# Optimization experiments

Measured on AMD Instinct MI355X. Metric: run time of the kernel, lower is better.

## Reference

```python
import jax, jax.numpy as jnp
import numpy as np

B, JX, JQ, D = 16, 4096, 512, 256
VERY_NEG = -1e30


def setup_inputs() -> dict:
    key = jax.random.key(0)
    ks = jax.random.split(key, 8)
    c = jax.random.normal(ks[0], (B, JX, D), dtype=jnp.float32)
    q = jax.random.normal(ks[1], (B, JQ, D), dtype=jnp.float32)
    # glorot-ish scaled weights for [4d, d] projections
    s = 1.0 / np.sqrt(4 * D)
    Wr = jax.random.normal(ks[2], (4 * D, D), dtype=jnp.float32) * s
    Wg = jax.random.normal(ks[3], (4 * D, D), dtype=jnp.float32) * s
    Br = jnp.zeros((D,), dtype=jnp.float32)
    Bg = jnp.zeros((D,), dtype=jnp.float32)
    # padding masks from random valid lengths (realistic ragged batch)
    c_len = jax.random.randint(ks[4], (B,), JX // 2, JX + 1)
    q_len = jax.random.randint(ks[5], (B,), JQ // 2, JQ + 1)
    c_mask = jnp.arange(JX)[None, :] < c_len[:, None]
    q_mask = jnp.arange(JQ)[None, :] < q_len[:, None]
    return {"c": c, "q": q, "Wr": Wr, "Br": Br, "Wg": Wg, "Bg": Bg,
            "c_mask": c_mask, "q_mask": q_mask}


def reference(c, q, Wr, Br, Wg, Bg, c_mask, q_mask):
    # logits[b,x,j] = <c[b,x], q[b,j]>
    logits = jnp.einsum('bxd,bjd->bxj', c, q)
    # exp_mask: add VERY_NEG where (c_mask & q_mask) is False
    cq_mask = c_mask[:, :, None] & q_mask[:, None, :]  # [B,JX,JQ]
    logits = logits + (1.0 - cq_mask.astype(logits.dtype)) * VERY_NEG
    a = jax.nn.softmax(logits, axis=-1)                # [B,JX,JQ]
    q_a = jnp.einsum('bxj,bjd->bxd', a, q)             # [B,JX,D]
    # semantic fusion unit
    cc = jnp.concatenate([c, q_a, c * q_a, c - q_a], axis=-1)  # [B,JX,4D]
    r_ = jnp.tanh(cc @ Wr + Br)
    g = jax.nn.sigmoid(cc @ Wg + Bg)
    return g * r_ + (1.0 - g) * c
```

## Files before the change

### kernel.cpp

```cpp
#include <hip/hip_runtime.h>
#include <hip/hip_bf16.h>
#include <stdint.h>

#define NB 16
#define JXX 4096
#define JQQ 512
#define DDD 256
#define LOG2E 1.44269504f

typedef __attribute__((ext_vector_type(8))) _Float16 f16x8;
typedef __attribute__((ext_vector_type(4))) _Float16 f16x4;
typedef __attribute__((ext_vector_type(4))) float f32x4;

__device__ __forceinline__ uint16_t f2h(float f) {
    union { _Float16 h; uint16_t s; } u; u.h = (_Float16)f; return u.s;
}
__device__ __forceinline__ float h2f(uint16_t s) {
    union { _Float16 h; uint16_t s; } u; u.s = s; return (float)u.h;
}

__device__ __forceinline__ void gload_lds16(const void* g, void* l) {
    __builtin_amdgcn_global_load_lds(
        (const __attribute__((address_space(1))) void*)g,
        (__attribute__((address_space(3))) void*)l, 16, 0, 0);
}

#define VMW(N) asm volatile("s_waitcnt vmcnt(" #N ")" ::: "memory")

__global__ void k_mask(const void* cmask, const void* qmask,
                       uint8_t* cm8, uint8_t* qm8) {
    int i = blockIdx.x * 256 + threadIdx.x;
    uint32_t w0c = *(const uint32_t*)cmask;
    uint32_t w0q = *(const uint32_t*)qmask;
    int mc = (w0c == 1u) ? 1 : (w0c == 0x3f800000u ? 2 : 0);
    int mq = (w0q == 1u) ? 1 : (w0q == 0x3f800000u ? 2 : 0);
    if (i < NB * JXX) {
        uint8_t v;
        if (mc == 1)      v = ((const int*)cmask)[i] != 0;
        else if (mc == 2) v = ((const float*)cmask)[i] != 0.0f;
        else              v = ((const uint8_t*)cmask)[i] != 0;
        cm8[i] = v;
    }
    if (i < NB * JQQ) {
        uint8_t v;
        if (mq == 1)      v = ((const int*)qmask)[i] != 0;
        else if (mq == 2) v = ((const float*)qmask)[i] != 0.0f;
        else              v = ((const uint8_t*)qmask)[i] != 0;
        qm8[i] = v;
    }
}

__global__ void k_prep_q(const float* __restrict__ qg,
                         uint16_t* __restrict__ qS,
                         uint16_t* __restrict__ qTS) {
    __shared__ float tile[64][65];
    const int b = blockIdx.z, j0 = blockIdx.x * 64, d0 = blockIdx.y * 64;
    const int t = threadIdx.x;
    #pragma unroll
    for (int i = 0; i < 16; i++) {
        int e = t + 256 * i;
        int r = e >> 6, c = e & 63;
        tile[r][c] = qg[((long)b * JQQ + j0 + r) * DDD + d0 + c];
    }
    __syncthreads();
    #pragma unroll
    for (int i = 0; i < 2; i++) {
        int e = t + 256 * i;
        int r = e >> 3, c8 = e & 7;
        f16x8 v;
        #pragma unroll
        for (int k = 0; k < 8; k++) v[k] = (_Float16)tile[r][c8 * 8 + k];
        int jt = (j0 >> 5) + (r >> 5);
        int row = r & 31;
        int d8 = (d0 >> 3) + c8;
        int byt = ((row * 512 + d8 * 16) ^ ((row & 7) << 4));
        *(f16x8*)(qS + ((long)(b * 16 + jt)) * 8192 + (byt >> 1)) = v;
    }
    #pragma unroll
    for (int i = 0; i < 2; i++) {
        int e = t + 256 * i;
        int dd = e >> 3, j8 = e & 7;
        f16x8 v;
        #pragma unroll
        for (int k = 0; k < 8; k++) v[k] = (_Float16)tile[j8 * 8 + k][dd];
        int jt = (j0 >> 5) + (j8 >> 2);
        int d = d0 + dd;
        int byt = ((d * 64 + (j8 & 3) * 16) ^ (((d >> 1) & 3) << 4));
        *(f16x8*)(qTS + ((long)(b * 16 + jt)) * 8192 + (byt >> 1)) = v;
    }
}

__global__ void k_prep_w(const float* __restrict__ Wr, const float* __restrict__ Wg,
                         uint16_t* __restrict__ WP2) {
    __shared__ _Float16 tile[32 * 264];
    const int rg = blockIdx.y;
    const float* W = rg ? Wg : Wr;
    const int kt = blockIdx.x, t = threadIdx.x;
    #pragma unroll
    for (int i = 0; i < 32; i++) {
        int e = t + 256 * i;
        int r = e >> 8, c = e & 255;
        tile[r * 264 + c] = (_Float16)W[(long)(kt * 32 + r) * 256 + c];
    }
    __syncthreads();
    const int step = (kt & 7) * 4 + (kt >> 3);
    #pragma unroll
    for (int ss = 0; ss < 4; ss++) {
        int slot = ss * 256 + t;
        int ntg = slot >> 6, lane = slot & 63;
        int gg = lane >> 4, l = lane & 15;
        f16x8 v;
        #pragma unroll
        for (int i = 0; i < 8; i++) v[i] = tile[(gg * 8 + i) * 264 + ntg * 16 + l];
        int hh = ntg >> 3, ntl = ntg & 7;
        long off = (long)step * 16384 + hh * 8192 + rg * 4096 + ntl * 512 + lane * 8;
        *(f16x8*)(WP2 + off) = v;
    }
}

__global__ __launch_bounds__(256, 2) void k_attn(
    const float* __restrict__ cg,
    const uint16_t* __restrict__ qS,
    const uint16_t* __restrict__ qTS,
    const uint8_t* __restrict__ cm8,
    const uint8_t* __restrict__ qm8,
    uint16_t* __restrict__ qa16,
    uint16_t* __restrict__ c16)
{
    __shared__ __align__(16) uint16_t qbuf[2][8192];
    __shared__ __align__(16) uint16_t qTbuf[2][8192];
    __shared__ __align__(16) uint16_t P_lds[4 * 32 * 40];
    __shared__ __align__(16) uint32_t qm_lds[128];

    const int b = blockIdx.y;
    const int t = threadIdx.x;
    const int wave = t >> 6;
    const int lane = t & 63;
    const int l15 = lane & 15;
    const int g = lane >> 4;
    const int xw = blockIdx.x * 128 + wave * 32;

    if (t < 128) {
        uint32_t m = ((const uint32_t*)(qm8 + (long)b * JQQ))[t];
        qm_lds[t] = m;
    }

    f16x8 cfrag[2][8];
    bool cvalid[2];
    float m_run[2], s_run[2];
    #pragma unroll
    for (int xs = 0; xs < 2; xs++) {
        const long rowg = (long)b * JXX + xw + xs * 16 + l15;
        const float* crow = cg + rowg * DDD;
        uint16_t* c16row = c16 + rowg * DDD;
        #pragma unroll
        for (int kb = 0; kb < 8; kb++) {
            float4 v0 = *(const float4*)(crow + kb * 32 + g * 8);
            float4 v1 = *(const float4*)(crow + kb * 32 + g * 8 + 4);
            f16x8 f;
            f[0] = (_Float16)v0.x; f[1] = (_Float16)v0.y; f[2] = (_Float16)v0.z; f[3] = (_Float16)v0.w;
            f[4] = (_Float16)v1.x; f[5] = (_Float16)v1.y; f[6] = (_Float16)v1.z; f[7] = (_Float16)v1.w;
            cfrag[xs][kb] = f;
            *(f16x8*)(c16row + kb * 32 + g * 8) = f;
        }
        cvalid[xs] = cm8[rowg] != 0;
        m_run[xs] = cvalid[xs] ? -1e30f : 0.0f;
        s_run[xs] = 0.0f;
    }
    const f32x4 fzero = {0.f, 0.f, 0.f, 0.f};
    f32x4 qa[16][2];
    #pragma unroll
    for (int i = 0; i < 16; i++) { qa[i][0] = fzero; qa[i][1] = fzero; }

    const uint16_t* qSb  = qS  + (long)(b * 16) * 8192;
    const uint16_t* qTSb = qTS + (long)(b * 16) * 8192;

    const int kbit = (l15 >> 2) & 1;
    const int qbase = l15 * 256 + (((g * 16) ^ ((l15 & 3) << 4)) >> 1);
    const int qTbase = l15 * 32 + ((g ^ ((l15 >> 1) & 3)) * 8);

    #define STAGE_ATTN(bsel, tile)                                              \
        {                                                                       \
            const uint16_t* s1 = qSb + (long)(tile) * 8192;                     \
            const uint16_t* s2 = qTSb + (long)(tile) * 8192;                    \
            _Pragma("unroll")                                                   \
            for (int i = 0; i < 4; i++)                                         \
                gload_lds16(s1 + i * 2048 + t * 8,                              \
                            &qbuf[bsel][i * 2048 + wave * 512]);                \
            _Pragma("unroll")                                                   \
            for (int i = 0; i < 4; i++)                                         \
                gload_lds16(s2 + i * 2048 + t * 8,                              \
                            &qTbuf[bsel][i * 2048 + wave * 512]);               \
        }

    STAGE_ATTN(0, 0);
    asm volatile("s_waitcnt lgkmcnt(0)" ::: "memory");
    __builtin_amdgcn_s_barrier();

    int cur = 0;
    for (int jt = 0; jt < 16; jt++) {
        if (jt < 15) {
            STAGE_ATTN(cur ^ 1, jt + 1);
            VMW(8);
        } else {
            VMW(0);
        }
        __builtin_amdgcn_s_barrier();
        __builtin_amdgcn_sched_barrier(0);

        const uint16_t* qb_l  = &qbuf[cur][0];
        const uint16_t* qTb_l = &qTbuf[cur][0];

        uint32_t qmw[2];
        qmw[0] = qm_lds[jt * 8 + g];
        qmw[1] = qm_lds[jt * 8 + 4 + g];

        f32x4 acc[2][2];
        acc[0][0] = fzero; acc[0][1] = fzero; acc[1][0] = fzero; acc[1][1] = fzero;
        #pragma unroll
        for (int js = 0; js < 2; js++) {
            #pragma unroll
            for (int kb = 0; kb < 8; kb++) {
                f16x8 qf = *(const f16x8*)(qb_l + js * 4096 + qbase + ((kb ^ kbit) << 5));
                acc[js][0] = __builtin_amdgcn_mfma_f32_16x16x32_f16(qf, cfrag[0][kb], acc[js][0], 0, 0, 0);
                acc[js][1] = __builtin_amdgcn_mfma_f32_16x16x32_f16(qf, cfrag[1][kb], acc[js][1], 0, 0, 0);
            }
        }

        f16x4 pv[2][2];
        float fsc[2];
        #pragma unroll
        for (int xs = 0; xs < 2; xs++) {
            float lmax = -1e30f;
            #pragma unroll
            for (int js = 0; js < 2; js++) {
                #pragma unroll
                for (int r = 0; r < 4; r++) {
                    bool qv = (qmw[js] >> (8 * r)) & 0xffu;
                    lmax = fmaxf(lmax, qv ? acc[js][xs][r] : -1e30f);
                }
            }
            lmax = fmaxf(lmax, __shfl_xor(lmax, 16));
            lmax = fmaxf(lmax, __shfl_xor(lmax, 32));
            float m_new = cvalid[xs] ? fmaxf(m_run[xs], lmax) : 0.0f;
            fsc[xs] = exp2f((m_run[xs] - m_new) * LOG2E);
            float psum = 0.0f;
            #pragma unroll
            for (int js = 0; js < 2; js++) {
                #pragma unroll
                for (int r = 0; r < 4; r++) {
                    bool qv = (qmw[js] >> (8 * r)) & 0xffu;
                    float p = qv ? exp2f((acc[js][xs][r] - m_new) * LOG2E) : 0.0f;
                    if (!cvalid[xs]) p = 1.0f;
                    psum += p;
                    pv[xs][js][r] = (_Float16)p;
                }
            }
            s_run[xs] = s_run[xs] * fsc[xs] + psum;
            m_run[xs] = m_new;
        }
        if (!__all(fsc[0] == 1.0f && fsc[1] == 1.0f)) {
            #pragma unroll
            for (int dt = 0; dt < 16; dt++) {
                #pragma unroll
                for (int xs = 0; xs < 2; xs++) {
                    qa[dt][xs][0] *= fsc[xs]; qa[dt][xs][1] *= fsc[xs];
                    qa[dt][xs][2] *= fsc[xs]; qa[dt][xs][3] *= fsc[xs];
                }
            }
        }

        uint16_t* Pw0 = P_lds + wave * 1280;
        #pragma unroll
        for (int xs = 0; xs < 2; xs++) {
            *(f16x4*)(Pw0 + (xs * 16 + l15) * 40 + g * 4) = pv[xs][0];
            *(f16x4*)(Pw0 + (xs * 16 + l15) * 40 + 16 + g * 4) = pv[xs][1];
        }
        f16x8 pa[2];
        pa[0] = *(const f16x8*)(Pw0 + l15 * 40 + g * 8);
        pa[1] = *(const f16x8*)(Pw0 + (16 + l15) * 40 + g * 8);

        #pragma unroll
        for (int dt = 0; dt < 16; dt++) {
            f16x8 bq = *(const f16x8*)(qTb_l + qTbase + dt * 512);
            qa[dt][0] = __builtin_amdgcn_mfma_f32_16x16x32_f16(bq, pa[0], qa[dt][0], 0, 0, 0);
            qa[dt][1] = __builtin_amdgcn_mfma_f32_16x16x32_f16(bq, pa[1], qa[dt][1], 0, 0, 0);
        }

        __builtin_amdgcn_sched_barrier(0);
        __builtin_amdgcn_s_barrier();
        cur ^= 1;
    }
    #undef STAGE_ATTN

    #pragma unroll
    for (int xs = 0; xs < 2; xs++) {
        float s_tot = s_run[xs] + __shfl_xor(s_run[xs], 16);
        s_tot = s_tot + __shfl_xor(s_tot, 32);
        float inv = 1.0f / s_tot;
        uint16_t* outp = qa16 + ((long)b * JXX + xw + xs * 16 + l15) * DDD;
        #pragma unroll
        for (int dt = 0; dt < 16; dt++) {
            f16x4 v;
            v[0] = (_Float16)(qa[dt][xs][0] * inv);
            v[1] = (_Float16)(qa[dt][xs][1] * inv);
            v[2] = (_Float16)(qa[dt][xs][2] * inv);
            v[3] = (_Float16)(qa[dt][xs][3] * inv);
            *(f16x4*)(outp + dt * 16 + g * 4) = v;
        }
    }
}

__global__ __launch_bounds__(256, 2) void k_sfu(
    const uint16_t* __restrict__ c16g,
    const uint16_t* __restrict__ qa16,
    const uint16_t* __restrict__ WP2,
    const float* __restrict__ Brb,
    const float* __restrict__ Bgb,
    float* __restrict__ outg)
{
    __shared__ __align__(16) uint16_t ab_lds[2][4096];
    __shared__ __align__(16) uint16_t wbuf[3][8192];

    const int t = threadIdx.x;
    const int wave = t >> 6, lane = t & 63;
    const int l15 = lane & 15, g = lane >> 4;
    const int mw = wave & 1, nw = wave >> 1;
    const long m0 = (long)blockIdx.x * 64;
    const int h = blockIdx.y, n0 = h * 128;

    const uint16_t* WPh = WP2 + (long)h * 8192;

    const f32x4 fzero = {0.f, 0.f, 0.f, 0.f};
    f32x4 accR[2][4], accG[2][4];
    #pragma unroll
    for (int a = 0; a < 2; a++)
        #pragma unroll
        for (int bq = 0; bq < 4; bq++) { accR[a][bq] = fzero; accG[a][bq] = fzero; }

    #define STAGE_CQA(dt_)                                                        \
        { _Pragma("unroll")                                                       \
          for (int j = 0; j < 2; j++) {                                           \
              int pp = j * 256 + t;                                               \
              int row = pp >> 3, pc = pp & 7;                                     \
              long src = (m0 + row) * 256 + (dt_) * 64 + ((pc ^ (row & 7)) << 3); \
              int dst = (j * 256 + wave * 64) * 8;                                \
              gload_lds16(c16g + src, &ab_lds[0][dst]);                           \
              gload_lds16(qa16 + src, &ab_lds[1][dst]);                           \
          } }

    #define STAGE_W(sidx_)                                                        \
        { _Pragma("unroll")                                                       \
          for (int i = 0; i < 4; i++) {                                           \
              int s = i * 4 + wave;                                               \
              gload_lds16(WPh + (long)(sidx_) * 16384 + s * 512 + lane * 8,       \
                          &wbuf[(sidx_) % 3][i * 2048 + wave * 512]);             \
          } }

    STAGE_CQA(0);
    STAGE_W(0);
    STAGE_W(1);
    VMW(8);
    __builtin_amdgcn_s_barrier();

    #pragma unroll
    for (int dt = 0; dt < 4; dt++) {
        #pragma unroll
        for (int kb = 0; kb < 2; kb++) {
            f16x8 af[4][2];
            #pragma unroll
            for (int mf = 0; mf < 2; mf++) {
                int row = mw * 32 + mf * 16 + l15;
                int c8 = kb * 4 + g;
                int off = row * 64 + ((c8 ^ (row & 7)) << 3);
                f16x8 cf = *(const f16x8*)(&ab_lds[0][off]);
                f16x8 qf = *(const f16x8*)(&ab_lds[1][off]);
                af[0][mf] = cf;
                af[1][mf] = qf;
                af[2][mf] = cf * qf;
                af[3][mf] = cf - qf;
            }
            #pragma unroll
            for (int comp = 0; comp < 4; comp++) {
                const int sidx = (dt * 2 + kb) * 4 + comp;
                if (dt < 3 && kb == 1 && comp == 1) STAGE_CQA(dt + 1);
                if (sidx <= 29) STAGE_W(sidx + 2);
                if (sidx <= 29) {
                    if (dt < 3 && kb == 1 && (comp == 1 || comp == 2)) { VMW(12); }
                    else { VMW(8); }
                } else if (sidx == 30) { VMW(4); }
                else { VMW(0); }
                __builtin_amdgcn_s_barrier();
                __builtin_amdgcn_sched_barrier(0);
                const uint16_t* Wb = &wbuf[sidx % 3][0];
                #pragma unroll
                for (int nt = 0; nt < 4; nt++) {
                    f16x8 br = *(const f16x8*)(Wb + (nw * 4 + nt) * 512 + lane * 8);
                    f16x8 bg = *(const f16x8*)(Wb + 4096 + (nw * 4 + nt) * 512 + lane * 8);
                    accR[0][nt] = __builtin_amdgcn_mfma_f32_16x16x32_f16(af[comp][0], br, accR[0][nt], 0, 0, 0);
                    accR[1][nt] = __builtin_amdgcn_mfma_f32_16x16x32_f16(af[comp][1], br, accR[1][nt], 0, 0, 0);
                    accG[0][nt] = __builtin_amdgcn_mfma_f32_16x16x32_f16(af[comp][0], bg, accG[0][nt], 0, 0, 0);
                    accG[1][nt] = __builtin_amdgcn_mfma_f32_16x16x32_f16(af[comp][1], bg, accG[1][nt], 0, 0, 0);
                }
                __builtin_amdgcn_sched_barrier(0);
                __builtin_amdgcn_s_barrier();
            }
        }
    }
    #undef STAGE_W
    #undef STAGE_CQA

    #pragma unroll
    for (int nt = 0; nt < 4; nt++) {
        int n = n0 + nw * 64 + nt * 16 + l15;
        float br = Brb[n], bg = Bgb[n];
        #pragma unroll
        for (int mf = 0; mf < 2; mf++) {
            long rowb = m0 + mw * 32 + mf * 16 + g * 4;
            #pragma unroll
            for (int r = 0; r < 4; r++) {
                float pr = accR[mf][nt][r] + br;
                float pg = accG[mf][nt][r] + bg;
                float x = fminf(fmaxf(pr, -30.f), 30.f);
                float e2 = __expf(2.f * x);
                float rr = (e2 - 1.f) / (e2 + 1.f);
                float gv = 1.0f / (1.0f + __expf(-pg));
                float cv = h2f(c16g[(rowb + r) * DDD + n]);
                outg[(rowb + r) * DDD + n] = gv * rr + (1.f - gv) * cv;
            }
        }
    }
}

extern "C" void kernel_launch(void* const* d_in, const int* in_sizes, int n_in,
                              void* d_out, int out_size, void* d_ws, size_t ws_size,
                              hipStream_t stream) {
    const float* c  = (const float*)d_in[0];
    const float* q  = (const float*)d_in[1];
    const float* Wr = (const float*)d_in[2];
    const float* Br = (const float*)d_in[3];
    const float* Wg = (const float*)d_in[4];
    const float* Bg = (const float*)d_in[5];
    const void* cmask = d_in[6];
    const void* qmask = d_in[7];

    char* ws = (char*)d_ws;
    uint16_t* qS    = (uint16_t*)(ws + 0);
    uint16_t* qTS   = (uint16_t*)(ws + 4194304);
    uint16_t* qa16  = (uint16_t*)(ws + 8388608);
    uint16_t* c16   = (uint16_t*)(ws + 41943040);
    uint16_t* WP2   = (uint16_t*)(ws + 75497472);
    uint8_t*  cm8   = (uint8_t*)(ws + 77594624);
    uint8_t*  qm8   = (uint8_t*)(ws + 77660160);
    (void)in_sizes; (void)n_in; (void)out_size; (void)ws_size;

    k_mask<<<dim3((NB * JXX + 255) / 256), dim3(256), 0, stream>>>(cmask, qmask, cm8, qm8);
    k_prep_q<<<dim3(8, 4, NB), dim3(256), 0, stream>>>(q, qS, qTS);
    k_prep_w<<<dim3(32, 2), dim3(256), 0, stream>>>(Wr, Wg, WP2);
    k_attn<<<dim3(JXX / 128, NB), dim3(256), 0, stream>>>(c, qS, qTS, cm8, qm8, qa16, c16);
    k_sfu<<<dim3((NB * JXX) / 64, 2), dim3(256), 0, stream>>>(
        c16, qa16, WP2, Br, Bg, (float*)d_out);
}
```

Before: 171.0 us.

## Load SFU operands directly from global memory and double block size

Removes the LDS staging, async global-to-LDS copies and per-step barriers from the semantic-fusion GEMM kernel. Each wave now reads its c/q_a fragments and weight fragments straight from global memory into registers. Blocks grow to 512 threads covering 128 rows, so more waves share each weight tile through the cache. This removes barrier and LDS overhead but relies on L1/L2 to serve repeated weight reads, and exposes global-load latency directly before each MFMA.

```diff
diff --git a/kernel.cpp b/kernel.cpp
--- a/kernel.cpp
+++ b/kernel.cpp
@@ -311,7 +311,7 @@
     }
 }
 
-__global__ __launch_bounds__(256, 2) void k_sfu(
+__global__ __launch_bounds__(512, 2) void k_sfu(
     const uint16_t* __restrict__ c16g,
     const uint16_t* __restrict__ qa16,
     const uint16_t* __restrict__ WP2,
@@ -319,17 +319,16 @@
     const float* __restrict__ Bgb,
     float* __restrict__ outg)
 {
-    __shared__ __align__(16) uint16_t ab_lds[2][4096];
-    __shared__ __align__(16) uint16_t wbuf[3][8192];
-
     const int t = threadIdx.x;
     const int wave = t >> 6, lane = t & 63;
     const int l15 = lane & 15, g = lane >> 4;
-    const int mw = wave & 1, nw = wave >> 1;
-    const long m0 = (long)blockIdx.x * 64;
+    const int mw = wave & 3, nw = wave >> 2;
+    const long m0 = (long)blockIdx.x * 128;
     const int h = blockIdx.y, n0 = h * 128;
 
-    const uint16_t* WPh = WP2 + (long)h * 8192;
+    const uint16_t* WPh = WP2 + (long)h * 8192 + (nw * 4) * 512 + lane * 8;
+    const uint16_t* cb = c16g + (m0 + mw * 32 + l15) * 256 + g * 8;
+    const uint16_t* qb = qa16 + (m0 + mw * 32 + l15) * 256 + g * 8;
 
     const f32x4 fzero = {0.f, 0.f, 0.f, 0.f};
     f32x4 accR[2][4], accG[2][4];
@@ -338,77 +337,42 @@
         #pragma unroll
         for (int bq = 0; bq < 4; bq++) { accR[a][bq] = fzero; accG[a][bq] = fzero; }
 
-    #define STAGE_CQA(dt_)                                                        \
-        { _Pragma("unroll")                                                       \
-          for (int j = 0; j < 2; j++) {                                           \
-              int pp = j * 256 + t;                                               \
-              int row = pp >> 3, pc = pp & 7;                                     \
-              long src = (m0 + row) * 256 + (dt_) * 64 + ((pc ^ (row & 7)) << 3); \
-              int dst = (j * 256 + wave * 64) * 8;                                \
-              gload_lds16(c16g + src, &ab_lds[0][dst]);                           \
-              gload_lds16(qa16 + src, &ab_lds[1][dst]);                           \
-          } }
-
-    #define STAGE_W(sidx_)                                                        \
-        { _Pragma("unroll")                                                       \
-          for (int i = 0; i < 4; i++) {                                           \
-              int s = i * 4 + wave;                                               \
-              gload_lds16(WPh + (long)(sidx_) * 16384 + s * 512 + lane * 8,       \
-                          &wbuf[(sidx_) % 3][i * 2048 + wave * 512]);             \
-          } }
-
-    STAGE_CQA(0);
-    STAGE_W(0);
-    STAGE_W(1);
-    VMW(8);
-    __builtin_amdgcn_s_barrier();
-
     #pragma unroll
     for (int dt = 0; dt < 4; dt++) {
+        f16x8 cf[2][2], qf[2][2];
+        #pragma unroll
+        for (int kb = 0; kb < 2; kb++)
+            #pragma unroll
+            for (int mf = 0; mf < 2; mf++) {
+                cf[kb][mf] = *(const f16x8*)(cb + mf * 4096 + dt * 64 + kb * 32);
+                qf[kb][mf] = *(const f16x8*)(qb + mf * 4096 + dt * 64 + kb * 32);
+            }
         #pragma unroll
         for (int kb = 0; kb < 2; kb++) {
             f16x8 af[4][2];
             #pragma unroll
             for (int mf = 0; mf < 2; mf++) {
-                int row = mw * 32 + mf * 16 + l15;
-                int c8 = kb * 4 + g;
-                int off = row * 64 + ((c8 ^ (row & 7)) << 3);
-                f16x8 cf = *(const f16x8*)(&ab_lds[0][off]);
-                f16x8 qf = *(const f16x8*)(&ab_lds[1][off]);
-                af[0][mf] = cf;
-                af[1][mf] = qf;
-                af[2][mf] = cf * qf;
-                af[3][mf] = cf - qf;
+                af[0][mf] = cf[kb][mf];
+                af[1][mf] = qf[kb][mf];
+                af[2][mf] = cf[kb][mf] * qf[kb][mf];
+                af[3][mf] = cf[kb][mf] - qf[kb][mf];
             }
             #pragma unroll
             for (int comp = 0; comp < 4; comp++) {
-                const int sidx = (dt * 2 + kb) * 4 + comp;
-                if (dt < 3 && kb == 1 && comp == 1) STAGE_CQA(dt + 1);
-                if (sidx <= 29) STAGE_W(sidx + 2);
-                if (sidx <= 29) {
-                    if (dt < 3 && kb == 1 && (comp == 1 || comp == 2)) { VMW(12); }
-                    else { VMW(8); }
-                } else if (sidx == 30) { VMW(4); }
-                else { VMW(0); }
-                __builtin_amdgcn_s_barrier();
-                __builtin_amdgcn_sched_barrier(0);
-                const uint16_t* Wb = &wbuf[sidx % 3][0];
+                const int s = (dt * 2 + kb) * 4 + comp;
+                const uint16_t* Wst = WPh + (long)s * 16384;
                 #pragma unroll
                 for (int nt = 0; nt < 4; nt++) {
-                    f16x8 br = *(const f16x8*)(Wb + (nw * 4 + nt) * 512 + lane * 8);
-                    f16x8 bg = *(const f16x8*)(Wb + 4096 + (nw * 4 + nt) * 512 + lane * 8);
+                    f16x8 br = *(const f16x8*)(Wst + nt * 512);
+                    f16x8 bg = *(const f16x8*)(Wst + 4096 + nt * 512);
                     accR[0][nt] = __builtin_amdgcn_mfma_f32_16x16x32_f16(af[comp][0], br, accR[0][nt], 0, 0, 0);
                     accR[1][nt] = __builtin_amdgcn_mfma_f32_16x16x32_f16(af[comp][1], br, accR[1][nt], 0, 0, 0);
                     accG[0][nt] = __builtin_amdgcn_mfma_f32_16x16x32_f16(af[comp][0], bg, accG[0][nt], 0, 0, 0);
                     accG[1][nt] = __builtin_amdgcn_mfma_f32_16x16x32_f16(af[comp][1], bg, accG[1][nt], 0, 0, 0);
                 }
-                __builtin_amdgcn_sched_barrier(0);
-                __builtin_amdgcn_s_barrier();
-            }
-        }
-    }
-    #undef STAGE_W
-    #undef STAGE_CQA
+            }
+        }
+    }
 
     #pragma unroll
     for (int nt = 0; nt < 4; nt++) {
@@ -458,6 +422,6 @@
     k_prep_q<<<dim3(8, 4, NB), dim3(256), 0, stream>>>(q, qS, qTS);
     k_prep_w<<<dim3(32, 2), dim3(256), 0, stream>>>(Wr, Wg, WP2);
     k_attn<<<dim3(JXX / 128, NB), dim3(256), 0, stream>>>(c, qS, qTS, cm8, qm8, qa16, c16);
-    k_sfu<<<dim3((NB * JXX) / 64, 2), dim3(256), 0, stream>>>(
+    k_sfu<<<dim3((NB * JXX) / 128, 2), dim3(512), 0, stream>>>(
         c16, qa16, WP2, Br, Bg, (float*)d_out);
 }
```

Result: slower. 288.1 us (+68.4%).
